# Performance work log

Hardware: AMD Instinct MI355X
Metric: run time of the kernel (lower is better)

## Reference

```python
import jax, jax.numpy as jnp
import numpy as np
from jax import lax

B, C, N, NB = 64, 512, 1024, 4
BC = C // NB
KS = [3, 5, 7, 9]
LEVEL = 2  # min(2, pywt.dwt_max_level(1024, 8)) = 2
FL = 8  # db4 filter length
DN = ('NCH', 'OIH', 'NCH')
# pywt db4 decomposition filters
DEC_LO = jnp.array([-0.010597401784997278, 0.032883011666982945, 0.030841381835986965,
                    -0.18703481171888114, -0.02798376941698385, 0.6308807679295904,
                    0.7148465705525415, 0.23037781330885523], jnp.float32)
DEC_HI = jnp.array([-0.23037781330885523, 0.7148465705525415, -0.6308807679295904,
                    -0.02798376941698385, 0.18703481171888114, 0.030841381835986965,
                    -0.032883011666982945, -0.010597401784997278], jnp.float32)


def conv1d(x, w, b, pad):
    y = lax.conv_general_dilated(x, w, (1,), [(pad, pad)], dimension_numbers=DN)
    return y + b[None, :, None]


def bn_relu(x, g, beta, eps=1e-5):
    # BatchNorm1d in train mode: batch statistics over (B, L) per channel
    mu = x.mean(axis=(0, 2), keepdims=True)
    var = ((x - mu) ** 2).mean(axis=(0, 2), keepdims=True)
    xn = (x - mu) * lax.rsqrt(var + eps)
    return jax.nn.relu(xn * g[None, :, None] + beta[None, :, None])


def dwt1d(x):
    # single-level pywt-compatible DWT, symmetric mode. x: [B, C, n]
    b, c, n = x.shape
    out = (n + FL - 1) // 2
    p = 2 * (out - 1) - n + FL
    xp = jnp.pad(x, ((0, 0), (0, 0), (p // 2, p - p // 2)), mode='symmetric')
    k = jnp.stack([DEC_LO[::-1], DEC_HI[::-1]])[:, None, :]  # [2,1,FL]
    y = lax.conv_general_dilated(xp.reshape(b * c, 1, -1), k, (2,), 'VALID',
                                 dimension_numbers=DN)
    y = y.reshape(b, c, 2, out)
    return y[:, :, 0], y[:, :, 1]  # (cA, cD)


def idwt1d(lo, hi):
    # single-level inverse DWT; output length = 2*nc - FL + 2
    b, c, nc = lo.shape
    x = jnp.stack([lo, hi], axis=2).reshape(b * c, 2, nc)
    # rec filters = dec filters reversed, so flipped-for-conv == dec filters
    k = jnp.stack([DEC_LO, DEC_HI])[None, :, :]  # [1,2,FL]
    y = lax.conv_general_dilated(x, k, (1,), [(FL - 1, FL - 1)],
                                 lhs_dilation=(2,), dimension_numbers=DN)
    y = y[:, 0, FL - 2: FL - 2 + 2 * nc - FL + 2]
    return y.reshape(b, c, -1)


def decouple(x):
    # TemporalPatternDecoupling: db4 wavedec(level=2) -> reconstruct low-pass-only
    # (long term) and detail-only (short term). Torch detaches before pywt.
    x = lax.stop_gradient(x)
    n = x.shape[-1]
    a, details = x, []
    for _ in range(LEVEL):
        a, d = dwt1d(a)
        details.append(d)
    la, sa = a, jnp.zeros_like(a)
    for d in reversed(details):
        dl = d.shape[-1]
        la = idwt1d(la[..., :dl], jnp.zeros_like(d))
        sa = idwt1d(sa[..., :dl], d)
    return sa[..., :n], la[..., :n]


def setup_inputs() -> dict:
    key = jax.random.key(0)
    ks = jax.random.split(key, 32)
    s = 0.05
    inp = {
        'x': jax.random.normal(ks[0], (B, C, N), jnp.float32),
        'w_init': jax.random.normal(ks[1], (C, C, 1), jnp.float32) * s,
        'b_init': jnp.zeros((C,), jnp.float32),
        'w_pf': jax.random.normal(ks[2], (BC, 2 * BC, 1), jnp.float32) * s,
        'b_pf': jnp.zeros((BC,), jnp.float32),
        'w_fus': jax.random.normal(ks[3], (C, C, 1), jnp.float32) * s,
        'b_fus': jnp.zeros((C,), jnp.float32),
    }
    for i in range(NB):
        inp[f'w_b{i + 1}'] = jax.random.normal(ks[4 + i], (BC, BC, KS[i]), jnp.float32) * s
        inp[f'b_b{i + 1}'] = jnp.zeros((BC,), jnp.float32)
        inp[f'g_b{i + 1}'] = jnp.ones((BC,), jnp.float32)
        inp[f'be_b{i + 1}'] = jnp.zeros((BC,), jnp.float32)
    return inp


def reference(x, w_init, b_init, w_b1, b_b1, g_b1, be_b1, w_b2, b_b2, g_b2, be_b2,
              w_b3, b_b3, g_b3, be_b3, w_b4, b_b4, g_b4, be_b4, w_pf, b_pf,
              w_fus, b_fus):
    identity = x
    h = conv1d(x, w_init, b_init, 0)
    branch_in = jnp.split(h, NB, axis=1)
    wb = [w_b1, w_b2, w_b3, w_b4]
    bb = [b_b1, b_b2, b_b3, b_b4]
    gb = [g_b1, g_b2, g_b3, g_b4]
    beb = [be_b1, be_b2, be_b3, be_b4]
    shorts, longs = [], []
    for i in range(NB):
        y = bn_relu(conv1d(branch_in[i], wb[i], bb[i], KS[i] // 2), gb[i], beb[i])
        s, l = decouple(y)
        shorts.append(s)
        longs.append(l)
    for b in range(1, NB):
        shorts[b] = shorts[b] + shorts[b - 1]
    for b in range(NB - 2, -1, -1):
        longs[b] = longs[b] + longs[b + 1]
    enhanced = [conv1d(jnp.concatenate([shorts[b], longs[b]], axis=1), w_pf, b_pf, 0)
                for b in range(NB)]
    out = conv1d(jnp.concatenate(enhanced, axis=1), w_fus, b_fus, 0)
    return out + identity
```

## Files before the change

kernel.cpp:

```cpp
#include <hip/hip_runtime.h>

typedef float  f32x4 __attribute__((ext_vector_type(4)));
typedef short  s16x8 __attribute__((ext_vector_type(8)));
typedef short  s16x4 __attribute__((ext_vector_type(4)));
typedef unsigned short u16;

struct PtrQuad { const float* p[4]; };

__constant__ float c_lo[8] = {-0.010597401784997278f, 0.032883011666982945f,
                              0.030841381835986965f, -0.18703481171888114f,
                              -0.02798376941698385f, 0.6308807679295904f,
                              0.7148465705525415f,  0.23037781330885523f};
__constant__ float c_hi[8] = {-0.23037781330885523f, 0.7148465705525415f,
                              -0.6308807679295904f, -0.02798376941698385f,
                              0.18703481171888114f, 0.030841381835986965f,
                              -0.032883011666982945f, -0.010597401784997278f};

__device__ __forceinline__ u16 f2bf(float f) {
    unsigned u = __float_as_uint(f);
    u += 0x7fffu + ((u >> 16) & 1u);
    return (u16)(u >> 16);
}
__device__ __forceinline__ float bf2f(u16 h) {
    return __uint_as_float(((unsigned)h) << 16);
}
__device__ __forceinline__ int lds_chunk(int row, int g) {
    return row * 4 + (g ^ ((row >> 1) & 3));
}
__device__ __forceinline__ void gload16(void* lds, const void* g) {
    __builtin_amdgcn_global_load_lds(
        (__attribute__((address_space(1))) const void*)g,
        (__attribute__((address_space(3))) void*)lds,
        16, 0, 0);
}
__device__ __forceinline__ void pipe_wait2(int t, int nt) {
    if (t + 1 < nt) asm volatile("s_waitcnt vmcnt(4)" ::: "memory");
    else            asm volatile("s_waitcnt vmcnt(0)" ::: "memory");
    __builtin_amdgcn_s_barrier();
    __builtin_amdgcn_sched_barrier(0);
}
__device__ __forceinline__ void pipe_endbar() {
    __builtin_amdgcn_sched_barrier(0);
    __builtin_amdgcn_s_barrier();
}

__global__ __launch_bounds__(256) void gemm_nt_k(
    const u16* __restrict__ A, long aB, int lda,
    const u16* __restrict__ B, long bB, int ldb,
    int K,
    u16* __restrict__ D, long dB, int dj,
    const float* __restrict__ bias)
{
    __shared__ s16x8 As[2 * 512];
    __shared__ s16x8 Bs[2 * 512];
    int flat = blockIdx.x + 8 * (blockIdx.y + 4 * blockIdx.z);
    int swz = (flat & 7) * 256 + (flat >> 3);
    const int j0 = (swz & 7) * 128;
    const int i0 = ((swz >> 3) & 3) * 128;
    const long bb = swz >> 5;
    const u16* Ab = A + bb * aB;
    const u16* Bb = B + bb * bB;
    const int tid = threadIdx.x;
    const int srow = tid >> 2, sg = tid & 3;
    const int ssg = sg ^ ((srow >> 1) & 3);
    const int l = tid & 63, w = tid >> 6;
    const int wi = (w >> 1) * 64, wj = (w & 1) * 64;
    const int lr = l & 15, lg = l >> 4;
    const long aoff0 = (long)(i0 + srow) * lda + ssg * 8;
    const long aoff1 = (long)(i0 + srow + 64) * lda + ssg * 8;
    const long boff0 = (long)(j0 + srow) * ldb + ssg * 8;
    const long boff1 = (long)(j0 + srow + 64) * ldb + ssg * 8;
    const int nt = K >> 5;
    auto stage = [&](int buf, int t) {
        const int k0 = t << 5;
        char* a0 = (char*)As + buf * 8192 + w * 1024;
        char* b0 = (char*)Bs + buf * 8192 + w * 1024;
        gload16(a0, Ab + aoff0 + k0);
        gload16(a0 + 4096, Ab + aoff1 + k0);
        gload16(b0, Bb + boff0 + k0);
        gload16(b0 + 4096, Bb + boff1 + k0);
    };
    f32x4 acc[4][4] = {};
    stage(0, 0);
    for (int t = 0; t < nt; ++t) {
        const int cur = t & 1;
        if (t + 1 < nt) stage(cur ^ 1, t + 1);
        pipe_wait2(t, nt);
        s16x8 af[4], bf[4];
        #pragma unroll
        for (int f = 0; f < 4; ++f) {
            af[f] = As[cur * 512 + lds_chunk(wi + f * 16 + lr, lg)];
            bf[f] = Bs[cur * 512 + lds_chunk(wj + f * 16 + lr, lg)];
        }
        __builtin_amdgcn_s_setprio(1);
        #pragma unroll
        for (int fi = 0; fi < 4; ++fi)
            #pragma unroll
            for (int fj = 0; fj < 4; ++fj)
                acc[fi][fj] = __builtin_amdgcn_mfma_f32_16x16x32_bf16(af[fi], bf[fj], acc[fi][fj], 0, 0, 0);
        __builtin_amdgcn_s_setprio(0);
        pipe_endbar();
    }
    u16* Db = D + bb * dB;
    #pragma unroll
    for (int fi = 0; fi < 4; ++fi) {
        const int i = i0 + wi + fi * 16 + lg * 4;
        float b0 = 0, b1 = 0, b2v = 0, b3 = 0;
        if (bias) { b0 = bias[i]; b1 = bias[i + 1]; b2v = bias[i + 2]; b3 = bias[i + 3]; }
        #pragma unroll
        for (int fj = 0; fj < 4; ++fj) {
            const int j = j0 + wj + fj * 16 + lr;
            f32x4 d = acc[fi][fj];
            s16x4 o;
            o[0] = (short)f2bf(d[0] + b0); o[1] = (short)f2bf(d[1] + b1);
            o[2] = (short)f2bf(d[2] + b2v); o[3] = (short)f2bf(d[3] + b3);
            *(s16x4*)(Db + (long)j * dj + i) = o;
        }
    }
}

__global__ __launch_bounds__(256) void gemm_branch4_k(
    const u16* __restrict__ WpAll,
    const u16* __restrict__ H,
    u16* __restrict__ Y,
    const u16* __restrict__ zbuf,
    float* __restrict__ part)
{
    __shared__ char Alds[2 * 8192];
    __shared__ char Blds[2 * 12288];
    __shared__ float sred[2][128];
    __shared__ float qred[2][128];
    int flat = blockIdx.x + 8 * (blockIdx.y + 4 * blockIdx.z);
    int swz = (flat & 7) * 256 + (flat >> 3);
    const int jblk = swz & 7;
    const int br = (swz >> 3) & 3;
    const long bb = swz >> 5;
    const int j0 = jblk * 128;
    const int taps = 3 + 2 * br;
    const int pad = 1 + br;
    const u16* Wpb = WpAll + (long)(br * br + 2 * br) * 16384;
    const u16* Hb = H + bb * 524288 + 128 * br;
    const int tid = threadIdx.x;
    const int l = tid & 63, w = tid >> 6;
    const int wi = (w >> 1) * 64, wj = (w & 1) * 64;
    const int lr = l & 15, lg = l >> 4;
    const int lrow = l >> 2, lq = l & 3;
    const int ssg2 = lq ^ ((lrow >> 1) & 3);
    const int lda = taps * 128;

    auto stageA = [&](int buf, int c, int t) {
        char* dst = Alds + buf * 8192 + w * 2048;
        #pragma unroll
        for (int q = 0; q < 2; ++q) {
            int row = w * 32 + q * 16 + lrow;
            gload16(dst + q * 1024,
                    Wpb + (long)row * lda + t * 128 + c * 32 + ssg2 * 8);
        }
    };
    auto stageB = [&](int buf, int c) {
        char* dst = Blds + buf * 12288 + w * 3072;
        #pragma unroll
        for (int q = 0; q < 3; ++q) {
            int winrow = w * 48 + q * 16 + lrow;
            int grow = j0 - 32 + winrow;
            const u16* src = (grow >= 0 && grow < 1024)
                           ? (Hb + (long)grow * 512 + c * 32 + ssg2 * 8) : zbuf;
            gload16(dst + q * 1024, src);
        }
    };

    f32x4 acc[4][4] = {};
    int abuf = 0, bbuf = 0;
    stageB(0, 0);
    stageA(0, 0, 0);
    for (int c = 0; c < 4; ++c) {
        for (int t = 0; t < taps; ++t) {
            if (t + 1 < taps) {
                stageA(abuf ^ 1, c, t + 1);
                asm volatile("s_waitcnt vmcnt(2)" ::: "memory");
            } else if (c + 1 < 4) {
                stageB(bbuf ^ 1, c + 1);
                stageA(abuf ^ 1, c + 1, 0);
                asm volatile("s_waitcnt vmcnt(5)" ::: "memory");
            } else {
                asm volatile("s_waitcnt vmcnt(0)" ::: "memory");
            }
            __builtin_amdgcn_s_barrier();
            __builtin_amdgcn_sched_barrier(0);
            const char* Al = Alds + abuf * 8192;
            const char* Bl = Blds + bbuf * 12288;
            const int shift2 = t - pad + 32;
            s16x8 af[4], bf[4];
            #pragma unroll
            for (int f = 0; f < 4; ++f) {
                int arow = wi + f * 16 + lr;
                af[f] = *(const s16x8*)(Al + arow * 64 + (lg ^ ((arow >> 1) & 3)) * 16);
                int brow = wj + f * 16 + lr + shift2;
                bf[f] = *(const s16x8*)(Bl + brow * 64 + (lg ^ ((brow >> 1) & 3)) * 16);
            }
            __builtin_amdgcn_s_setprio(1);
            #pragma unroll
            for (int fi = 0; fi < 4; ++fi)
                #pragma unroll
                for (int fj = 0; fj < 4; ++fj)
                    acc[fi][fj] = __builtin_amdgcn_mfma_f32_16x16x32_bf16(af[fi], bf[fj], acc[fi][fj], 0, 0, 0);
            __builtin_amdgcn_s_setprio(0);
            __builtin_amdgcn_sched_barrier(0);
            __builtin_amdgcn_s_barrier();
            abuf ^= 1;
            if (t == taps - 1) bbuf ^= 1;
        }
    }
    u16* Db = Y + bb * 524288 + 128 * br;
    #pragma unroll
    for (int fi = 0; fi < 4; ++fi) {
        const int i = wi + fi * 16 + lg * 4;
        #pragma unroll
        for (int fj = 0; fj < 4; ++fj) {
            const int j = j0 + wj + fj * 16 + lr;
            f32x4 d = acc[fi][fj];
            s16x4 o;
            o[0] = (short)f2bf(d[0]); o[1] = (short)f2bf(d[1]);
            o[2] = (short)f2bf(d[2]); o[3] = (short)f2bf(d[3]);
            *(s16x4*)(Db + (long)j * 512 + i) = o;
        }
    }
    float sv[16], qv[16];
    #pragma unroll
    for (int fi = 0; fi < 4; ++fi)
        #pragma unroll
        for (int e = 0; e < 4; ++e) {
            float s = 0.f, q = 0.f;
            #pragma unroll
            for (int fj = 0; fj < 4; ++fj) { float d = acc[fi][fj][e]; s += d; q += d * d; }
            sv[fi * 4 + e] = s; qv[fi * 4 + e] = q;
        }
    #pragma unroll
    for (int m = 1; m < 16; m <<= 1) {
        #pragma unroll
        for (int r = 0; r < 16; ++r) {
            sv[r] += __shfl_xor(sv[r], m, 64);
            qv[r] += __shfl_xor(qv[r], m, 64);
        }
    }
    __syncthreads();
    if (lr == 0) {
        #pragma unroll
        for (int r = 0; r < 16; ++r) {
            int co = wi + (r >> 2) * 16 + lg * 4 + (r & 3);
            sred[w & 1][co] = sv[r];
            qred[w & 1][co] = qv[r];
        }
    }
    __syncthreads();
    if (tid < 128) {
        long blk = (long)br * 512 + bb * 8 + jblk;
        part[blk * 256 + tid]       = sred[0][tid] + sred[1][tid];
        part[blk * 256 + 128 + tid] = qred[0][tid] + qred[1][tid];
    }
}

__global__ __launch_bounds__(256) void gemm_psl_k(
    const u16* __restrict__ Ybn,
    const u16* __restrict__ Bmat,
    u16* __restrict__ PSL)
{
    __shared__ s16x8 As[2 * 512];
    __shared__ s16x8 Bs[2 * 512];
    int flat = blockIdx.x + 8 * (blockIdx.y + 8 * blockIdx.z);
    int swz = (flat & 7) * 512 + (flat >> 3);
    const int j0 = (swz & 7) * 128;
    const int i0 = ((swz >> 3) & 7) * 128;
    const long bb = swz >> 6;
    const int tid = threadIdx.x;
    const u16* Ab = Ybn + bb * 524288;
    const int srow = tid >> 2, sg = tid & 3;
    const int ssg = sg ^ ((srow >> 1) & 3);
    const int l = tid & 63, w = tid >> 6;
    const int wi = (w >> 1) * 64, wj = (w & 1) * 64;
    const int lr = l & 15, lg = l >> 4;
    const long aoff0 = (long)(i0 + srow) * 512 + ssg * 8;
    const long aoff1 = (long)(i0 + srow + 64) * 512 + ssg * 8;
    const long boff0 = (long)(j0 + srow) * 512 + ssg * 8;
    const long boff1 = (long)(j0 + srow + 64) * 512 + ssg * 8;
    const int nt = 16;
    auto stage = [&](int buf, int t) {
        const int k0 = t << 5;
        char* a0 = (char*)As + buf * 8192 + w * 1024;
        char* b0 = (char*)Bs + buf * 8192 + w * 1024;
        gload16(a0, Ab + aoff0 + k0);
        gload16(a0 + 4096, Ab + aoff1 + k0);
        gload16(b0, Bmat + boff0 + k0);
        gload16(b0 + 4096, Bmat + boff1 + k0);
    };
    f32x4 acc[4][4] = {};
    stage(0, 0);
    for (int t = 0; t < nt; ++t) {
        const int cur = t & 1;
        if (t + 1 < nt) stage(cur ^ 1, t + 1);
        pipe_wait2(t, nt);
        s16x8 af[4], bf[4];
        #pragma unroll
        for (int f = 0; f < 4; ++f) {
            af[f] = As[cur * 512 + lds_chunk(wi + f * 16 + lr, lg)];
            bf[f] = Bs[cur * 512 + lds_chunk(wj + f * 16 + lr, lg)];
        }
        __builtin_amdgcn_s_setprio(1);
        #pragma unroll
        for (int fi = 0; fi < 4; ++fi)
            #pragma unroll
            for (int fj = 0; fj < 4; ++fj)
                acc[fi][fj] = __builtin_amdgcn_mfma_f32_16x16x32_bf16(af[fi], bf[fj], acc[fi][fj], 0, 0, 0);
        __builtin_amdgcn_s_setprio(0);
        pipe_endbar();
    }
    u16* Db = PSL + bb * 1048576;
    #pragma unroll
    for (int fi = 0; fi < 4; ++fi) {
        const int i = i0 + wi + fi * 16 + lg * 4;
        #pragma unroll
        for (int fj = 0; fj < 4; ++fj) {
            const int j = j0 + wj + fj * 16 + lr;
            f32x4 d = acc[fi][fj];
            s16x4 o;
            o[0] = (short)f2bf(d[0]); o[1] = (short)f2bf(d[1]);
            o[2] = (short)f2bf(d[2]); o[3] = (short)f2bf(d[3]);
            *(s16x4*)(Db + (long)j * 1024 + i) = o;
        }
    }
}

__global__ __launch_bounds__(256) void gemm_time_k(
    const u16* __restrict__ MS,
    const u16* __restrict__ PSL,
    const float* __restrict__ b2, const float* __restrict__ X,
    float* __restrict__ OUT)
{
    __shared__ s16x8 As[2 * 512];
    __shared__ s16x8 Bs[2 * 512];
    int flat = blockIdx.x + 4 * (blockIdx.y + 8 * blockIdx.z);
    int swz = (flat & 7) * 256 + (flat >> 3);
    const int j0 = (swz & 3) * 128;
    const int i0 = ((swz >> 2) & 7) * 128;
    const long bb = swz >> 5;
    const int tid = threadIdx.x;
    const int srow = tid >> 2, sg = tid & 3;
    const int ssg = sg ^ ((srow >> 1) & 3);
    const int l = tid & 63, w = tid >> 6;
    const int wi = (w >> 1) * 64, wj = (w & 1) * 64;
    const int lr = l & 15, lg = l >> 4;
    const int klo = (i0 - 32) > 0 ? (i0 - 32) : 0;
    const int khi = (i0 + 160) < 1024 ? (i0 + 160) : 1024;
    const int nt = (khi - klo) >> 5;
    const u16* B = PSL + bb * 1048576;
    auto stage = [&](int buf, int t) {
        const int k0 = klo + (t << 5);
        char* a0 = (char*)As + buf * 8192 + w * 1024;
        char* b0 = (char*)Bs + buf * 8192 + w * 1024;
        gload16(a0, MS + (long)(i0 + srow) * 1024 + k0 + ssg * 8);
        gload16(a0 + 4096, MS + (long)(i0 + srow + 64) * 1024 + k0 + ssg * 8);
        gload16(b0, B + (long)(j0 + srow) * 1024 + k0 + ssg * 8);
        gload16(b0 + 4096, B + (long)(j0 + srow + 64) * 1024 + k0 + ssg * 8);
    };
    f32x4 acc[4][4] = {};
    stage(0, 0);
    for (int t = 0; t < nt; ++t) {
        const int cur = t & 1;
        if (t + 1 < nt) stage(cur ^ 1, t + 1);
        pipe_wait2(t, nt);
        s16x8 af[4], bf[4];
        #pragma unroll
        for (int f = 0; f < 4; ++f) {
            af[f] = As[cur * 512 + lds_chunk(wi + f * 16 + lr, lg)];
            bf[f] = Bs[cur * 512 + lds_chunk(wj + f * 16 + lr, lg)];
        }
        __builtin_amdgcn_s_setprio(1);
        #pragma unroll
        for (int fi = 0; fi < 4; ++fi)
            #pragma unroll
            for (int fj = 0; fj < 4; ++fj)
                acc[fi][fj] = __builtin_amdgcn_mfma_f32_16x16x32_bf16(af[fi], bf[fj], acc[fi][fj], 0, 0, 0);
        __builtin_amdgcn_s_setprio(0);
        pipe_endbar();
    }
    float* Ob = OUT + bb * 524288;
    const float* Xb = X + bb * 524288;
    const u16* PLb = PSL + bb * 1048576 + 524288;
    #pragma unroll
    for (int fi = 0; fi < 4; ++fi) {
        const int i = i0 + wi + fi * 16 + lg * 4;
        #pragma unroll
        for (int fj = 0; fj < 4; ++fj) {
            const int j = j0 + wj + fj * 16 + lr;
            const long a = (long)j * 1024 + i;
            f32x4 d = acc[fi][fj];
            const float bj = b2[j];
            f32x4 xv = *(const f32x4*)(Xb + a);
            s16x4 pl4 = *(const s16x4*)(PLb + a);
            f32x4 o;
            o[0] = d[0] + bj + xv[0] + bf2f((u16)pl4[0]);
            o[1] = d[1] + bj + xv[1] + bf2f((u16)pl4[1]);
            o[2] = d[2] + bj + xv[2] + bf2f((u16)pl4[2]);
            o[3] = d[3] + bj + xv[3] + bf2f((u16)pl4[3]);
            *(f32x4*)(Ob + a) = o;
        }
    }
}

__global__ __launch_bounds__(256) void build_M_k(u16* __restrict__ MS)
{
    __shared__ float a1[515], d1[515], a2[261], d2[261], sa1[515];
    const int r = blockIdx.x;
    const int t = threadIdx.x;
    for (int m = t; m < 515; m += 256) {
        float sa = 0.f, sd = 0.f;
        #pragma unroll
        for (int j = 0; j < 8; ++j) {
            int tt = 2 * m + 1 - j;
            tt = (tt < 0) ? (-tt - 1) : tt;
            tt = (tt >= 1024) ? (2047 - tt) : tt;
            if (tt == r) { sa += c_lo[j]; sd += c_hi[j]; }
        }
        a1[m] = sa; d1[m] = sd;
    }
    __syncthreads();
    for (int m = t; m < 261; m += 256) {
        float sa = 0.f, sd = 0.f;
        #pragma unroll
        for (int j = 0; j < 8; ++j) {
            int tt = 2 * m + 1 - j;
            tt = (tt < 0) ? (-tt - 1) : tt;
            tt = (tt >= 515) ? (1029 - tt) : tt;
            float v = a1[tt];
            sa += v * c_lo[j]; sd += v * c_hi[j];
        }
        a2[m] = sa; d2[m] = sd;
    }
    __syncthreads();
    for (int m = t; m < 515; m += 256) {
        float ss = 0.f;
        #pragma unroll
        for (int k = 0; k < 8; ++k) {
            int tt = m + k - 1;
            if (tt & 1) continue;
            int j = tt >> 1;
            if (j < 0 || j >= 261) continue;
            ss += c_hi[k] * d2[j];
        }
        sa1[m] = ss;
    }
    __syncthreads();
    for (int n = t; n < 1024; n += 256) {
        float ss = 0.f;
        #pragma unroll
        for (int k = 0; k < 8; ++k) {
            int tt = n + k - 1;
            if (tt & 1) continue;
            int j = tt >> 1;
            if (j < 0 || j >= 515) continue;
            ss += c_lo[k] * sa1[j] + c_hi[k] * d1[j];
        }
        MS[(long)n * 1024 + r] = f2bf(ss);
    }
}

__global__ __launch_bounds__(256) void pack_weights_k(
    const float* __restrict__ wi,
    const float* __restrict__ b1, const float* __restrict__ b2_,
    const float* __restrict__ b3, const float* __restrict__ b4,
    u16* __restrict__ Wi, u16* __restrict__ Wp)
{
    int i = blockIdx.x * 256 + threadIdx.x;
    if (i < 262144) Wi[i] = f2bf(wi[i]);
    if (i < 393216) {
        int base, taps;
        const float* s;
        if (i < 49152)       { base = 0;      taps = 3; s = b1; }
        else if (i < 131072) { base = 49152;  taps = 5; s = b2_; }
        else if (i < 245760) { base = 131072; taps = 7; s = b3; }
        else                 { base = 245760; taps = 9; s = b4; }
        int rem = i - base;
        int stride = taps * 128;
        int co = rem / stride;
        int r2 = rem - co * stride;
        int tap = r2 >> 7, ci = r2 & 127;
        Wp[i] = f2bf(s[(long)(co * 128 + ci) * taps + tap]);
    }
}

__global__ __launch_bounds__(256) void make_Ucum_k(
    const float* __restrict__ wf, const float* __restrict__ wp,
    u16* __restrict__ UDUL)
{
    int gid = blockIdx.x * 256 + threadIdx.x;
    int co = gid >> 7, cc = gid & 127;
    float us[4], ul[4];
    #pragma unroll
    for (int b = 0; b < 4; ++b) {
        float s = 0.f, t = 0.f;
        for (int q = 0; q < 128; ++q) {
            float f = wf[(long)co * 512 + b * 128 + q];
            s += f * wp[q * 256 + cc];
            t += f * wp[q * 256 + 128 + cc];
        }
        us[b] = s; ul[b] = t;
    }
    float suf[4], pre[4];
    float acc = 0.f;
    for (int b = 3; b >= 0; --b) { acc += us[b]; suf[b] = acc; }
    acc = 0.f;
    for (int b = 0; b < 4; ++b) { acc += ul[b]; pre[b] = acc; }
    #pragma unroll
    for (int b = 0; b < 4; ++b) {
        UDUL[(long)co * 512 + b * 128 + cc]         = f2bf(suf[b] - pre[b]);
        UDUL[(long)(512 + co) * 512 + b * 128 + cc] = f2bf(pre[b]);
    }
}

__global__ __launch_bounds__(256) void make_bias2_k(
    const float* __restrict__ wf, const float* __restrict__ bpf,
    const float* __restrict__ bfus, float* __restrict__ b2)
{
    int co = blockIdx.x * 256 + threadIdx.x;
    if (co >= 512) return;
    float s = bfus[co];
    for (int j = 0; j < 512; ++j) s += wf[(long)co * 512 + j] * bpf[j & 127];
    b2[co] = s;
}

__global__ __launch_bounds__(256) void zero_k(float* __restrict__ p, int n)
{
    int i = blockIdx.x * 256 + threadIdx.x;
    if (i < n) p[i] = 0.f;
}

__global__ __launch_bounds__(256) void trX_k(const float* __restrict__ x, u16* __restrict__ xcl)
{
    __shared__ float sh[32][33];
    const int n0 = blockIdx.x * 32, c0 = blockIdx.y * 32;
    const long bb = blockIdx.z;
    const int tx = threadIdx.x, ty = threadIdx.y;
    const float* xb = x + bb * 524288;
    u16* ob = xcl + bb * 524288;
    #pragma unroll
    for (int k = 0; k < 4; ++k)
        sh[ty + 8 * k][tx] = xb[(long)(c0 + ty + 8 * k) * 1024 + n0 + tx];
    __syncthreads();
    #pragma unroll
    for (int k = 0; k < 4; ++k)
        ob[(long)(n0 + ty + 8 * k) * 512 + c0 + tx] = f2bf(sh[tx][ty + 8 * k]);
}

__global__ __launch_bounds__(256) void bn_coef_k(
    const float* __restrict__ part, PtrQuad g, PtrQuad be, float* __restrict__ scsh)
{
    __shared__ float rs[256], rq[256];
    int c = blockIdx.x;
    int br = c >> 7, cc = c & 127;
    const float* pb = part + (long)br * 131072;
    int t = threadIdx.x;
    float s = pb[(2 * t) * 256 + cc]       + pb[(2 * t + 1) * 256 + cc];
    float q = pb[(2 * t) * 256 + 128 + cc] + pb[(2 * t + 1) * 256 + 128 + cc];
    rs[t] = s; rq[t] = q;
    __syncthreads();
    for (int off = 128; off > 0; off >>= 1) {
        if (t < off) { rs[t] += rs[t + off]; rq[t] += rq[t + off]; }
        __syncthreads();
    }
    if (t == 0) {
        float mu = rs[0] * (1.0f / 65536.0f);
        float var = rq[0] * (1.0f / 65536.0f) - mu * mu;
        float sc = g.p[br][cc] * rsqrtf(var + 1e-5f);
        scsh[c] = sc;
        scsh[512 + c] = be.p[br][cc] - mu * sc;
    }
}

__global__ __launch_bounds__(256) void bn_apply_k(
    u16* __restrict__ Y, const float* __restrict__ scsh)
{
    __shared__ float sc_[512];
    __shared__ float sh_[512];
    const int t = threadIdx.x;
    #pragma unroll
    for (int q = 0; q < 2; ++q) {
        sc_[t + q * 256] = scsh[t + q * 256];
        sh_[t + q * 256] = scsh[512 + t + q * 256];
    }
    __syncthreads();
    long gid = (long)blockIdx.x * 256 + t;
    long r = gid >> 6; int cg = (int)(gid & 63);
    u16* p = Y + r * 512 + cg * 8;
    s16x8 v = *(const s16x8*)p;
    #pragma unroll
    for (int e = 0; e < 8; ++e) {
        int c = cg * 8 + e;
        float f = bf2f((u16)v[e]) * sc_[c] + sh_[c];
        v[e] = (short)f2bf(f > 0.f ? f : 0.f);
    }
    *(s16x8*)p = v;
}

extern "C" void kernel_launch(void* const* d_in, const int* in_sizes, int n_in,
                              void* d_out, int out_size, void* d_ws, size_t ws_size,
                              hipStream_t stream)
{
    const float* x      = (const float*)d_in[0];
    const float* w_init = (const float*)d_in[1];
    const float* b_init = (const float*)d_in[2];
    const float* w_pf   = (const float*)d_in[3];
    const float* b_pf   = (const float*)d_in[4];
    const float* w_fus  = (const float*)d_in[5];
    const float* b_fus  = (const float*)d_in[6];
    const float *w_b[4];
    PtrQuad g, be;
    for (int i = 0; i < 4; ++i) {
        w_b[i]  = (const float*)d_in[7 + 4 * i];
        g.p[i]  = (const float*)d_in[9 + 4 * i];
        be.p[i] = (const float*)d_in[10 + 4 * i];
    }
    float* outf = (float*)d_out;

    char* p = (char*)d_ws;
    u16* xcl   = (u16*)p;  p += 67108864;
    u16* h     = (u16*)p;  p += 67108864;
    u16* Y     = (u16*)p;  p += 67108864;
    u16* PSL   = (u16*)p;  p += 134217728;
    u16* Wi    = (u16*)p;  p += 524288;
    u16* Wp    = (u16*)p;  p += 786432;
    u16* UDUL  = (u16*)p;  p += 1048576;
    u16* MrowS = (u16*)p;  p += 2097152;
    float* b2  = (float*)p; p += 2048;
    float* zbuf= (float*)p; p += 256;
    float* scsh= (float*)p; p += 4096;
    float* part= (float*)p; p += 2097152;

    pack_weights_k<<<1536, 256, 0, stream>>>(w_init, w_b[0], w_b[1], w_b[2], w_b[3], Wi, Wp);
    make_Ucum_k<<<256, 256, 0, stream>>>(w_fus, w_pf, UDUL);
    make_bias2_k<<<2, 256, 0, stream>>>(w_fus, b_pf, b_fus, b2);
    build_M_k<<<1024, 256, 0, stream>>>(MrowS);
    zero_k<<<1, 256, 0, stream>>>(zbuf, 64);

    trX_k<<<dim3(32, 16, 64), dim3(32, 8), 0, stream>>>(x, xcl);

    gemm_nt_k<<<dim3(8, 4, 64), 256, 0, stream>>>(Wi, 0, 512, xcl, 524288, 512, 512,
                                                  h, 524288, 512, b_init);

    gemm_branch4_k<<<dim3(8, 4, 64), 256, 0, stream>>>(Wp, h, Y, (const u16*)zbuf, part);

    bn_coef_k<<<512, 256, 0, stream>>>(part, g, be, scsh);
    bn_apply_k<<<16384, 256, 0, stream>>>(Y, scsh);

    gemm_psl_k<<<dim3(8, 8, 64), 256, 0, stream>>>(Y, UDUL, PSL);

    gemm_time_k<<<dim3(4, 8, 64), 256, 0, stream>>>(MrowS, PSL, b2, x, outf);
}
```

Measured before the change: 476.5 us.

## Reassociate channel and time GEMMs to apply the time matrix before channel mixing

Reorders the matrix product chain. The banded time-operator matrix now multiplies the transposed BN output first, producing Z with 512 channels instead of a 1024-wide PSL. A final GEMM then accumulates Z·U_short and Y·U_long over two K passes, fused with the bias and residual add. BN-apply now also writes a transposed copy of Y, and the separate long-path readback is dropped. This cuts the intermediate buffer size and the FLOPs of the dense 1024-wide GEMM. In exchange it adds a transpose write and performs bf16 rounding at a different point.

After: 501.4 us. 5.2% more time.

```diff
diff --git a/kernel.cpp b/kernel.cpp
--- a/kernel.cpp
+++ b/kernel.cpp
@@ -260,38 +260,36 @@
     }
 }
 
-__global__ __launch_bounds__(256) void gemm_psl_k(
-    const u16* __restrict__ Ybn,
-    const u16* __restrict__ Bmat,
-    u16* __restrict__ PSL)
+__global__ __launch_bounds__(256) void gemm_z_k(
+    const u16* __restrict__ YT,
+    const u16* __restrict__ MS,
+    u16* __restrict__ Z)
 {
     __shared__ s16x8 As[2 * 512];
     __shared__ s16x8 Bs[2 * 512];
-    int flat = blockIdx.x + 8 * (blockIdx.y + 8 * blockIdx.z);
-    int swz = (flat & 7) * 512 + (flat >> 3);
+    int flat = blockIdx.x + 8 * (blockIdx.y + 4 * blockIdx.z);
+    int swz = (flat & 7) * 256 + (flat >> 3);
     const int j0 = (swz & 7) * 128;
-    const int i0 = ((swz >> 3) & 7) * 128;
-    const long bb = swz >> 6;
+    const int i0 = ((swz >> 3) & 3) * 128;
+    const long bb = swz >> 5;
+    const u16* Ab = YT + bb * 524288;
     const int tid = threadIdx.x;
-    const u16* Ab = Ybn + bb * 524288;
     const int srow = tid >> 2, sg = tid & 3;
     const int ssg = sg ^ ((srow >> 1) & 3);
     const int l = tid & 63, w = tid >> 6;
     const int wi = (w >> 1) * 64, wj = (w & 1) * 64;
     const int lr = l & 15, lg = l >> 4;
-    const long aoff0 = (long)(i0 + srow) * 512 + ssg * 8;
-    const long aoff1 = (long)(i0 + srow + 64) * 512 + ssg * 8;
-    const long boff0 = (long)(j0 + srow) * 512 + ssg * 8;
-    const long boff1 = (long)(j0 + srow + 64) * 512 + ssg * 8;
-    const int nt = 16;
+    const int klo = (j0 - 32) > 0 ? (j0 - 32) : 0;
+    const int khi = (j0 + 160) < 1024 ? (j0 + 160) : 1024;
+    const int nt = (khi - klo) >> 5;
     auto stage = [&](int buf, int t) {
-        const int k0 = t << 5;
+        const int k0 = klo + (t << 5);
         char* a0 = (char*)As + buf * 8192 + w * 1024;
         char* b0 = (char*)Bs + buf * 8192 + w * 1024;
-        gload16(a0, Ab + aoff0 + k0);
-        gload16(a0 + 4096, Ab + aoff1 + k0);
-        gload16(b0, Bmat + boff0 + k0);
-        gload16(b0 + 4096, Bmat + boff1 + k0);
+        gload16(a0, Ab + (long)(i0 + srow) * 1024 + k0 + ssg * 8);
+        gload16(a0 + 4096, Ab + (long)(i0 + srow + 64) * 1024 + k0 + ssg * 8);
+        gload16(b0, MS + (long)(j0 + srow) * 1024 + k0 + ssg * 8);
+        gload16(b0 + 4096, MS + (long)(j0 + srow + 64) * 1024 + k0 + ssg * 8);
     };
     f32x4 acc[4][4] = {};
     stage(0, 0);
@@ -314,7 +312,7 @@
         __builtin_amdgcn_s_setprio(0);
         pipe_endbar();
     }
-    u16* Db = PSL + bb * 1048576;
+    u16* Db = Z + bb * 524288;
     #pragma unroll
     for (int fi = 0; fi < 4; ++fi) {
         const int i = i0 + wi + fi * 16 + lg * 4;
@@ -325,14 +323,14 @@
             s16x4 o;
             o[0] = (short)f2bf(d[0]); o[1] = (short)f2bf(d[1]);
             o[2] = (short)f2bf(d[2]); o[3] = (short)f2bf(d[3]);
-            *(s16x4*)(Db + (long)j * 1024 + i) = o;
-        }
-    }
-}
-
-__global__ __launch_bounds__(256) void gemm_time_k(
-    const u16* __restrict__ MS,
-    const u16* __restrict__ PSL,
+            *(s16x4*)(Db + (long)j * 512 + i) = o;
+        }
+    }
+}
+
+__global__ __launch_bounds__(256) void gemm_out_k(
+    const u16* __restrict__ Z, const u16* __restrict__ Ybn,
+    const u16* __restrict__ UDUL,
     const float* __restrict__ b2, const float* __restrict__ X,
     float* __restrict__ OUT)
 {
@@ -349,18 +347,22 @@
     const int l = tid & 63, w = tid >> 6;
     const int wi = (w >> 1) * 64, wj = (w & 1) * 64;
     const int lr = l & 15, lg = l >> 4;
-    const int klo = (i0 - 32) > 0 ? (i0 - 32) : 0;
-    const int khi = (i0 + 160) < 1024 ? (i0 + 160) : 1024;
-    const int nt = (khi - klo) >> 5;
-    const u16* B = PSL + bb * 1048576;
+    const u16* A0 = Z + bb * 524288;
+    const u16* A1 = Ybn + bb * 524288;
+    const u16* B0 = UDUL;
+    const u16* B1 = UDUL + 262144;
+    const int nt = 32;
     auto stage = [&](int buf, int t) {
-        const int k0 = klo + (t << 5);
+        const int pass = t >> 4;
+        const int k0 = (t & 15) << 5;
+        const u16* A = pass ? A1 : A0;
+        const u16* B = pass ? B1 : B0;
         char* a0 = (char*)As + buf * 8192 + w * 1024;
         char* b0 = (char*)Bs + buf * 8192 + w * 1024;
-        gload16(a0, MS + (long)(i0 + srow) * 1024 + k0 + ssg * 8);
-        gload16(a0 + 4096, MS + (long)(i0 + srow + 64) * 1024 + k0 + ssg * 8);
-        gload16(b0, B + (long)(j0 + srow) * 1024 + k0 + ssg * 8);
-        gload16(b0 + 4096, B + (long)(j0 + srow + 64) * 1024 + k0 + ssg * 8);
+        gload16(a0, A + (long)(i0 + srow) * 512 + k0 + ssg * 8);
+        gload16(a0 + 4096, A + (long)(i0 + srow + 64) * 512 + k0 + ssg * 8);
+        gload16(b0, B + (long)(j0 + srow) * 512 + k0 + ssg * 8);
+        gload16(b0 + 4096, B + (long)(j0 + srow + 64) * 512 + k0 + ssg * 8);
     };
     f32x4 acc[4][4] = {};
     stage(0, 0);
@@ -385,7 +387,6 @@
     }
     float* Ob = OUT + bb * 524288;
     const float* Xb = X + bb * 524288;
-    const u16* PLb = PSL + bb * 1048576 + 524288;
     #pragma unroll
     for (int fi = 0; fi < 4; ++fi) {
         const int i = i0 + wi + fi * 16 + lg * 4;
@@ -396,12 +397,9 @@
             f32x4 d = acc[fi][fj];
             const float bj = b2[j];
             f32x4 xv = *(const f32x4*)(Xb + a);
-            s16x4 pl4 = *(const s16x4*)(PLb + a);
             f32x4 o;
-            o[0] = d[0] + bj + xv[0] + bf2f((u16)pl4[0]);
-            o[1] = d[1] + bj + xv[1] + bf2f((u16)pl4[1]);
-            o[2] = d[2] + bj + xv[2] + bf2f((u16)pl4[2]);
-            o[3] = d[3] + bj + xv[3] + bf2f((u16)pl4[3]);
+            o[0] = d[0] + bj + xv[0]; o[1] = d[1] + bj + xv[1];
+            o[2] = d[2] + bj + xv[2]; o[3] = d[3] + bj + xv[3];
             *(f32x4*)(Ob + a) = o;
         }
     }
@@ -576,29 +574,31 @@
     }
 }
 
-__global__ __launch_bounds__(256) void bn_apply_k(
-    u16* __restrict__ Y, const float* __restrict__ scsh)
-{
-    __shared__ float sc_[512];
-    __shared__ float sh_[512];
-    const int t = threadIdx.x;
-    #pragma unroll
-    for (int q = 0; q < 2; ++q) {
-        sc_[t + q * 256] = scsh[t + q * 256];
-        sh_[t + q * 256] = scsh[512 + t + q * 256];
-    }
-    __syncthreads();
-    long gid = (long)blockIdx.x * 256 + t;
-    long r = gid >> 6; int cg = (int)(gid & 63);
-    u16* p = Y + r * 512 + cg * 8;
-    s16x8 v = *(const s16x8*)p;
-    #pragma unroll
-    for (int e = 0; e < 8; ++e) {
-        int c = cg * 8 + e;
-        float f = bf2f((u16)v[e]) * sc_[c] + sh_[c];
-        v[e] = (short)f2bf(f > 0.f ? f : 0.f);
-    }
-    *(s16x8*)p = v;
+__global__ __launch_bounds__(256) void bn_apply_tr_k(
+    u16* __restrict__ Y, u16* __restrict__ YT, const float* __restrict__ scsh)
+{
+    __shared__ u16 sh[32][34];
+    __shared__ float sc_[32], shf_[32];
+    const int m0 = blockIdx.x * 32, c0 = blockIdx.y * 32;
+    const long bb = blockIdx.z;
+    const int tx = threadIdx.x, ty = threadIdx.y;
+    if (ty == 0) { sc_[tx] = scsh[c0 + tx]; shf_[tx] = scsh[512 + c0 + tx]; }
+    __syncthreads();
+    u16* Yb = Y + bb * 524288;
+    u16* Tb = YT + bb * 524288;
+    #pragma unroll
+    for (int k = 0; k < 4; ++k) {
+        int m = m0 + ty + 8 * k;
+        long a = (long)m * 512 + c0 + tx;
+        float f = bf2f(Yb[a]) * sc_[tx] + shf_[tx];
+        u16 o = f2bf(f > 0.f ? f : 0.f);
+        Yb[a] = o;
+        sh[ty + 8 * k][tx] = o;
+    }
+    __syncthreads();
+    #pragma unroll
+    for (int k = 0; k < 4; ++k)
+        Tb[(long)(c0 + ty + 8 * k) * 1024 + m0 + tx] = sh[tx][ty + 8 * k];
 }
 
 extern "C" void kernel_launch(void* const* d_in, const int* in_sizes, int n_in,
@@ -625,7 +625,8 @@
     u16* xcl   = (u16*)p;  p += 67108864;
     u16* h     = (u16*)p;  p += 67108864;
     u16* Y     = (u16*)p;  p += 67108864;
-    u16* PSL   = (u16*)p;  p += 134217728;
+    u16* YT    = (u16*)p;  p += 67108864;
+    u16* Z     = (u16*)p;  p += 67108864;
     u16* Wi    = (u16*)p;  p += 524288;
     u16* Wp    = (u16*)p;  p += 786432;
     u16* UDUL  = (u16*)p;  p += 1048576;
@@ -649,9 +650,9 @@
     gemm_branch4_k<<<dim3(8, 4, 64), 256, 0, stream>>>(Wp, h, Y, (const u16*)zbuf, part);
 
     bn_coef_k<<<512, 256, 0, stream>>>(part, g, be, scsh);
-    bn_apply_k<<<16384, 256, 0, stream>>>(Y, scsh);
-
-    gemm_psl_k<<<dim3(8, 8, 64), 256, 0, stream>>>(Y, UDUL, PSL);
-
-    gemm_time_k<<<dim3(4, 8, 64), 256, 0, stream>>>(MrowS, PSL, b2, x, outf);
-}
+    bn_apply_tr_k<<<dim3(32, 16, 64), dim3(32, 8), 0, stream>>>(Y, YT, scsh);
+
+    gemm_z_k<<<dim3(8, 4, 64), 256, 0, stream>>>(YT, MrowS, Z);
+
+    gemm_out_k<<<dim3(4, 8, 64), 256, 0, stream>>>(Z, Y, UDUL, b2, x, outf);
+}
```
